# Optimization experiments

Hardware: AMD Instinct MI355X
Metric: run time of the kernel (lower is better)

## Reference

```python
import jax, jax.numpy as jnp
import numpy as np

N_VERTS, N_RADIAL, N_ANGULAR, FEAT = 100000, 5, 8, 16
AMT_TEMPLATES, OUTPUT_DIM = 8, 32


def setup_inputs() -> dict:
    key = jax.random.key(0)
    k1, k2, k3, k4, k5, k6 = jax.random.split(key, 6)
    mesh_signal = jax.random.normal(k1, (N_VERTS, FEAT), dtype=jnp.float32)
    bary_weights = jax.random.uniform(k2, (N_VERTS, N_RADIAL, N_ANGULAR, 3), dtype=jnp.float32)
    interp_coeffs = jax.random.uniform(
        k3, (N_RADIAL, N_ANGULAR, N_RADIAL * N_ANGULAR), dtype=jnp.float32)
    template_weights = jax.random.normal(
        k4, (AMT_TEMPLATES, OUTPUT_DIM, FEAT), dtype=jnp.float32)
    bias = jax.random.normal(k5, (AMT_TEMPLATES, OUTPUT_DIM), dtype=jnp.float32)
    bary_indices = jax.random.randint(k6, (N_VERTS, N_RADIAL, N_ANGULAR, 3), 0, N_VERTS, dtype=jnp.int32)
    return {
        "mesh_signal": mesh_signal,
        "bary_weights": bary_weights,
        "interp_coeffs": interp_coeffs,
        "template_weights": template_weights,
        "bias": bias,
        "bary_indices": bary_indices,
    }


def reference(mesh_signal, bary_weights, interp_coeffs, template_weights, bias, bary_indices):
    n, R, A, _ = bary_indices.shape
    K = R * A
    # --- patch operator: barycentric gather + weighted interpolation ---
    gathered = mesh_signal[bary_indices]                         # (n, R, A, 3, F)
    interp = jnp.einsum('nrak,nrakf->nraf', bary_weights, gathered)  # (n, R, A, F)
    # --- prior: matvec with interpolation coefficients over flattened template ---
    flat = interp.reshape(n, K, -1)                              # (n, K, F)
    interp = jnp.einsum('nkf,rak->nraf', flat, interp_coeffs)    # (n, R, A, F)
    # --- fold: W @ X then reduce_sum over template-vertex axis. Since the
    # activation comes AFTER the reduce_sum, sum(W @ X, -1) == W @ sum(X, -1),
    # so we reduce first to avoid an (n, T, O, K) intermediate. ---
    s = interp.reshape(n, K, -1).sum(axis=1)                     # (n, F)
    pre = jnp.einsum('tof,nf->nto', template_weights, s) + bias  # (n, T, O)
    act = jax.nn.relu(pre)
    return act.sum(axis=1)                                       # (n, O)
```

## Files before the change

kernel.cpp:

```cpp
#include <hip/hip_runtime.h>

#define KK 40
#define M3 120
#define MM4 30
#define RCH 15
#define FEAT 16
#define NT 8
#define ODIM 32
#define VPB 32
#define BLOCK 256
#define SST 17

typedef unsigned int u32;
typedef unsigned short u16;
typedef float  f32x2 __attribute__((ext_vector_type(2)));
typedef float  f32x4 __attribute__((ext_vector_type(4)));
typedef int    i32x4 __attribute__((ext_vector_type(4)));
typedef u32    u32x4 __attribute__((ext_vector_type(4)));

__global__ void cs3_kernel(const float* __restrict__ ic, float* __restrict__ cs3) {
    __shared__ float cs[KK];
    const int t = threadIdx.x;
    if (t < KK) {
        float s = 0.f;
        #pragma unroll
        for (int ra = 0; ra < KK; ++ra) s += ic[ra * KK + t];
        cs[t] = s;
    }
    __syncthreads();
    if (t < M3) cs3[t] = cs[t / 3];
}

__device__ __forceinline__ u16 f2bf_rne(float x) {
    u32 u = __float_as_uint(x);
    u32 r = (u + 0x7fffu + ((u >> 16) & 1u)) >> 16;
    return (u16)r;
}

__global__ void cvt_kernel(const float* __restrict__ mesh, u16* __restrict__ mbf, int total) {
    const int i = blockIdx.x * blockDim.x + threadIdx.x;
    const int base = i * 8;
    if (base < total) {
        f32x4 a = __builtin_nontemporal_load((const f32x4*)(mesh + base));
        f32x4 b = __builtin_nontemporal_load((const f32x4*)(mesh + base + 4));
        u32x4 v;
        v.x = (u32)f2bf_rne(a.x) | ((u32)f2bf_rne(a.y) << 16);
        v.y = (u32)f2bf_rne(a.z) | ((u32)f2bf_rne(a.w) << 16);
        v.z = (u32)f2bf_rne(b.x) | ((u32)f2bf_rne(b.y) << 16);
        v.w = (u32)f2bf_rne(b.z) | ((u32)f2bf_rne(b.w) << 16);
        *(u32x4*)(mbf + base) = v;
    }
}

__device__ __forceinline__ void acc8(f32x2 acc2[4], const u32x4 g, const float s) {
    const f32x2 s2 = {s, s};
    f32x2 p;
    p.x = __uint_as_float(g.x << 16);
    p.y = __uint_as_float(g.x & 0xffff0000u);
    acc2[0] = __builtin_elementwise_fma(p, s2, acc2[0]);
    p.x = __uint_as_float(g.y << 16);
    p.y = __uint_as_float(g.y & 0xffff0000u);
    acc2[1] = __builtin_elementwise_fma(p, s2, acc2[1]);
    p.x = __uint_as_float(g.z << 16);
    p.y = __uint_as_float(g.z & 0xffff0000u);
    acc2[2] = __builtin_elementwise_fma(p, s2, acc2[2]);
    p.x = __uint_as_float(g.w << 16);
    p.y = __uint_as_float(g.w & 0xffff0000u);
    acc2[3] = __builtin_elementwise_fma(p, s2, acc2[3]);
}

__device__ __forceinline__ void gather4_sc0(const u32x4* p0, const u32x4* p1,
                                            const u32x4* p2, const u32x4* p3,
                                            u32x4& g0, u32x4& g1, u32x4& g2, u32x4& g3) {
    asm volatile(
        "global_load_dwordx4 %0, %4, off sc0\n\t"
        "global_load_dwordx4 %1, %5, off sc0\n\t"
        "global_load_dwordx4 %2, %6, off sc0\n\t"
        "global_load_dwordx4 %3, %7, off sc0\n\t"
        "s_waitcnt vmcnt(0)"
        : "=&v"(g0), "=&v"(g1), "=&v"(g2), "=&v"(g3)
        : "v"(p0), "v"(p1), "v"(p2), "v"(p3)
        : "memory");
}

__global__ __launch_bounds__(BLOCK, 8) void conv_kernel(
    const u16*   __restrict__ mbf,
    const float* __restrict__ bw,
    const float* __restrict__ W,
    const float* __restrict__ bias,
    const int*   __restrict__ bi,
    const float* __restrict__ cs3,
    float*       __restrict__ out,
    int n)
{
    __shared__ f32x4 s_buf[VPB * SST * 2];
    __shared__ float s_sig[VPB][FEAT + 1];

    f32x4* s_bw4 = s_buf;
    i32x4* s_bi4 = (i32x4*)(s_buf + VPB * SST);
    float (*s_out)[ODIM + 1] = (float(*)[ODIM + 1])s_buf;

    const int tid = threadIdx.x;
    const int vg0 = blockIdx.x * VPB;

    const f32x4* bw4g  = (const f32x4*)bw;
    const i32x4* bi4g  = (const i32x4*)bi;
    const f32x4* cs34g = (const f32x4*)cs3;

    const int vloc = tid >> 3;
    const int jc   = (tid >> 2) & 1;
    const int mc   = (tid >> 1) & 1;
    const int q    = tid & 1;
    const int vg   = vg0 + vloc;

    f32x2 acc2[4];
    #pragma unroll
    for (int e = 0; e < 4; ++e) acc2[e] = (f32x2){0.f, 0.f};

    #pragma unroll
    for (int r = 0; r < 2; ++r) {
        if (r) __syncthreads();

        #pragma unroll
        for (int ii = 0; ii < 2; ++ii) {
            const int i = tid + ii * BLOCK;
            if (i < VPB * RCH) {
                const int v = i / RCH;
                const int c = i - v * RCH;
                if (vg0 + v < n) {
                    const int gchunk = (vg0 + v) * MM4 + r * RCH + c;
                    f32x4 wv = __builtin_nontemporal_load(bw4g + gchunk);
                    i32x4 iv = __builtin_nontemporal_load(bi4g + gchunk);
                    const f32x4 cc = cs34g[r * RCH + c];
                    wv.x *= cc.x; wv.y *= cc.y; wv.z *= cc.z; wv.w *= cc.w;
                    s_bw4[v * SST + c] = wv;
                    s_bi4[v * SST + c] = iv;
                }
            }
        }
        __syncthreads();

        if (vg < n) {
            const int row   = vloc * SST;
            const int cbase = mc ? 8 : 0;
            #pragma unroll
            for (int b = 0; b < 4; ++b) {
                const int s0 = 2 * b;
                const int s1 = 2 * b + 1;
                const bool v0 = (mc == 0) || (s0 < 7);
                const bool v1 = (mc == 0) || (s1 < 7);
                const f32x4 wq0 = s_bw4[row + (v0 ? cbase + s0 : 0)];
                const i32x4 iq0 = s_bi4[row + (v0 ? cbase + s0 : 0)];
                const f32x4 wq1 = s_bw4[row + (v1 ? cbase + s1 : 0)];
                const i32x4 iq1 = s_bi4[row + (v1 ? cbase + s1 : 0)];
                const float wa0 = v0 ? (jc ? wq0.z : wq0.x) : 0.f;
                const float wa1 = v0 ? (jc ? wq0.w : wq0.y) : 0.f;
                const int   ia0 = v0 ? (jc ? iq0.z : iq0.x) : 0;
                const int   ia1 = v0 ? (jc ? iq0.w : iq0.y) : 0;
                const float wb0 = v1 ? (jc ? wq1.z : wq1.x) : 0.f;
                const float wb1 = v1 ? (jc ? wq1.w : wq1.y) : 0.f;
                const int   ib0 = v1 ? (jc ? iq1.z : iq1.x) : 0;
                const int   ib1 = v1 ? (jc ? iq1.w : iq1.y) : 0;

                u32x4 g0, g1, g2, g3;
                gather4_sc0((const u32x4*)(mbf + (size_t)ia0 * FEAT) + q,
                            (const u32x4*)(mbf + (size_t)ia1 * FEAT) + q,
                            (const u32x4*)(mbf + (size_t)ib0 * FEAT) + q,
                            (const u32x4*)(mbf + (size_t)ib1 * FEAT) + q,
                            g0, g1, g2, g3);

                acc8(acc2, g0, wa0);
                acc8(acc2, g1, wa1);
                acc8(acc2, g2, wb0);
                acc8(acc2, g3, wb1);
            }
        }
    }

    float a8[8] = { acc2[0].x, acc2[0].y, acc2[1].x, acc2[1].y,
                    acc2[2].x, acc2[2].y, acc2[3].x, acc2[3].y };
    #pragma unroll
    for (int e = 0; e < 8; ++e) a8[e] += __shfl_xor(a8[e], 4);
    #pragma unroll
    for (int e = 0; e < 8; ++e) a8[e] += __shfl_xor(a8[e], 2);

    if (jc == 0) {
        const f32x4 v = (mc == 0) ? (f32x4){a8[0], a8[1], a8[2], a8[3]}
                                  : (f32x4){a8[4], a8[5], a8[6], a8[7]};
        *(f32x4*)(&s_sig[vloc][q * 8 + mc * 4]) = v;
    }
    __syncthreads();

    {
        const int lane = tid & 63;
        const int wave = __builtin_amdgcn_readfirstlane(tid >> 6);
        const int v    = lane & (VPB - 1);

        float s[FEAT];
        #pragma unroll
        for (int f = 0; f < FEAT; ++f) s[f] = s_sig[v][f];

        float oacc[8];
        #pragma unroll
        for (int oi = 0; oi < 8; ++oi) oacc[oi] = 0.f;

        #pragma unroll 2
        for (int t = 0; t < NT; ++t) {
            #pragma unroll
            for (int oi = 0; oi < 8; ++oi) {
                const int o = wave * 8 + oi;
                float pre = bias[t * ODIM + o];
                const float* wrow = W + ((size_t)t * ODIM + o) * FEAT;
                #pragma unroll
                for (int f = 0; f < FEAT; ++f)
                    pre = fmaf(wrow[f], s[f], pre);
                oacc[oi] += fmaxf(pre, 0.f);
            }
        }

        if (lane < VPB) {
            #pragma unroll
            for (int oi = 0; oi < 8; ++oi)
                s_out[v][wave * 8 + oi] = oacc[oi];
        }
    }
    __syncthreads();

    {
        const int v   = tid >> 3;
        const int oq  = tid & 7;
        const int vgo = vg0 + v;
        if (vgo < n) {
            const f32x4 val = { s_out[v][oq * 4 + 0], s_out[v][oq * 4 + 1],
                                s_out[v][oq * 4 + 2], s_out[v][oq * 4 + 3] };
            *(f32x4*)(out + (size_t)vgo * ODIM + oq * 4) = val;
        }
    }
}

extern "C" void kernel_launch(void* const* d_in, const int* in_sizes, int n_in,
                              void* d_out, int out_size, void* d_ws, size_t ws_size,
                              hipStream_t stream) {
    const float* mesh = (const float*)d_in[0];
    const float* bw   = (const float*)d_in[1];
    const float* ic   = (const float*)d_in[2];
    const float* W    = (const float*)d_in[3];
    const float* bias = (const float*)d_in[4];
    const int*   bi   = (const int*)d_in[5];
    float* out = (float*)d_out;

    const int n = in_sizes[0] / FEAT;
    const int total = n * FEAT;

    float* cs3 = (float*)d_ws;
    u16*   mbf = (u16*)((char*)d_ws + 512);

    cs3_kernel<<<1, 128, 0, stream>>>(ic, cs3);

    const int cvt_threads = (total + 7) / 8;
    cvt_kernel<<<(cvt_threads + 255) / 256, 256, 0, stream>>>(mesh, mbf, total);

    const int blocks = (n + VPB - 1) / VPB;
    conv_kernel<<<blocks, BLOCK, 0, stream>>>(mbf, bw, W, bias, bi, cs3, out, n);
}
```

Baseline: 93.88 us.

## Software-pipeline gather batches and merge prep kernels into one launch

The gather loop becomes a double-buffered pipeline. Batch N+1 is issued before batch N is consumed, using s_waitcnt vmcnt(4) instead of waiting for all loads to finish, so memory latency overlaps with FMA work. The cs3 and bf16-conversion kernels are merged into one launch to save a kernel launch. Occupancy hint drops from 8 to 6 waves per SIMD to make room for the extra in-flight registers, which may reduce latency hiding across waves.

```diff
diff --git a/kernel.cpp b/kernel.cpp
--- a/kernel.cpp
+++ b/kernel.cpp
@@ -18,27 +18,28 @@
 typedef int    i32x4 __attribute__((ext_vector_type(4)));
 typedef u32    u32x4 __attribute__((ext_vector_type(4)));
 
-__global__ void cs3_kernel(const float* __restrict__ ic, float* __restrict__ cs3) {
-    __shared__ float cs[KK];
-    const int t = threadIdx.x;
-    if (t < KK) {
-        float s = 0.f;
-        #pragma unroll
-        for (int ra = 0; ra < KK; ++ra) s += ic[ra * KK + t];
-        cs[t] = s;
-    }
-    __syncthreads();
-    if (t < M3) cs3[t] = cs[t / 3];
-}
-
 __device__ __forceinline__ u16 f2bf_rne(float x) {
     u32 u = __float_as_uint(x);
     u32 r = (u + 0x7fffu + ((u >> 16) & 1u)) >> 16;
     return (u16)r;
 }
 
-__global__ void cvt_kernel(const float* __restrict__ mesh, u16* __restrict__ mbf, int total) {
-    const int i = blockIdx.x * blockDim.x + threadIdx.x;
+__global__ void prep_kernel(const float* __restrict__ mesh, const float* __restrict__ ic,
+                            u16* __restrict__ mbf, float* __restrict__ cs3, int total) {
+    const int t = threadIdx.x;
+    if (blockIdx.x == 0) {
+        __shared__ float cs[KK];
+        if (t < KK) {
+            float s = 0.f;
+            #pragma unroll
+            for (int ra = 0; ra < KK; ++ra) s += ic[ra * KK + t];
+            cs[t] = s;
+        }
+        __syncthreads();
+        if (t < M3) cs3[t] = cs[t / 3];
+        return;
+    }
+    const int i = (blockIdx.x - 1) * BLOCK + t;
     const int base = i * 8;
     if (base < total) {
         f32x4 a = __builtin_nontemporal_load((const f32x4*)(mesh + base));
@@ -69,21 +70,61 @@
     acc2[3] = __builtin_elementwise_fma(p, s2, acc2[3]);
 }
 
-__device__ __forceinline__ void gather4_sc0(const u32x4* p0, const u32x4* p1,
-                                            const u32x4* p2, const u32x4* p3,
-                                            u32x4& g0, u32x4& g1, u32x4& g2, u32x4& g3) {
+__device__ __forceinline__ void issue4_sc0(const u32x4* p0, const u32x4* p1,
+                                           const u32x4* p2, const u32x4* p3,
+                                           u32x4& g0, u32x4& g1, u32x4& g2, u32x4& g3) {
     asm volatile(
         "global_load_dwordx4 %0, %4, off sc0\n\t"
         "global_load_dwordx4 %1, %5, off sc0\n\t"
         "global_load_dwordx4 %2, %6, off sc0\n\t"
-        "global_load_dwordx4 %3, %7, off sc0\n\t"
-        "s_waitcnt vmcnt(0)"
+        "global_load_dwordx4 %3, %7, off sc0"
         : "=&v"(g0), "=&v"(g1), "=&v"(g2), "=&v"(g3)
         : "v"(p0), "v"(p1), "v"(p2), "v"(p3)
         : "memory");
 }
 
-__global__ __launch_bounds__(BLOCK, 8) void conv_kernel(
+#define WAIT_VM4() do { asm volatile("s_waitcnt vmcnt(4)" ::: "memory"); \
+                        __builtin_amdgcn_sched_barrier(0); } while (0)
+#define WAIT_VM0() do { asm volatile("s_waitcnt vmcnt(0)" ::: "memory"); \
+                        __builtin_amdgcn_sched_barrier(0); } while (0)
+
+struct GBatch { u32x4 g0, g1, g2, g3; float w0, w1, w2, w3; };
+
+__device__ __forceinline__ void prep_issue(GBatch& B,
+                                           const f32x4* __restrict__ s_bw4,
+                                           const i32x4* __restrict__ s_bi4,
+                                           int row, int cbase, int jc, int q, int mc, int b,
+                                           const u16* __restrict__ mbf) {
+    const int s0 = 2 * b, s1 = 2 * b + 1;
+    const bool v0 = (mc == 0) || (s0 < 7);
+    const bool v1 = (mc == 0) || (s1 < 7);
+    const f32x4 wq0 = s_bw4[row + cbase + (v0 ? s0 : 0)];
+    const i32x4 iq0 = s_bi4[row + cbase + (v0 ? s0 : 0)];
+    const f32x4 wq1 = s_bw4[row + cbase + (v1 ? s1 : 0)];
+    const i32x4 iq1 = s_bi4[row + cbase + (v1 ? s1 : 0)];
+    B.w0 = v0 ? (jc ? wq0.z : wq0.x) : 0.f;
+    B.w1 = v0 ? (jc ? wq0.w : wq0.y) : 0.f;
+    B.w2 = v1 ? (jc ? wq1.z : wq1.x) : 0.f;
+    B.w3 = v1 ? (jc ? wq1.w : wq1.y) : 0.f;
+    const int i0 = v0 ? (jc ? iq0.z : iq0.x) : 0;
+    const int i1 = v0 ? (jc ? iq0.w : iq0.y) : 0;
+    const int i2 = v1 ? (jc ? iq1.z : iq1.x) : 0;
+    const int i3 = v1 ? (jc ? iq1.w : iq1.y) : 0;
+    issue4_sc0((const u32x4*)(mbf + (size_t)i0 * FEAT) + q,
+               (const u32x4*)(mbf + (size_t)i1 * FEAT) + q,
+               (const u32x4*)(mbf + (size_t)i2 * FEAT) + q,
+               (const u32x4*)(mbf + (size_t)i3 * FEAT) + q,
+               B.g0, B.g1, B.g2, B.g3);
+}
+
+__device__ __forceinline__ void consume(f32x2 acc2[4], const GBatch& B) {
+    acc8(acc2, B.g0, B.w0);
+    acc8(acc2, B.g1, B.w1);
+    acc8(acc2, B.g2, B.w2);
+    acc8(acc2, B.g3, B.w3);
+}
+
+__global__ __launch_bounds__(BLOCK, 6) void conv_kernel(
     const u16*   __restrict__ mbf,
     const float* __restrict__ bw,
     const float* __restrict__ W,
@@ -143,37 +184,19 @@
         if (vg < n) {
             const int row   = vloc * SST;
             const int cbase = mc ? 8 : 0;
-            #pragma unroll
-            for (int b = 0; b < 4; ++b) {
-                const int s0 = 2 * b;
-                const int s1 = 2 * b + 1;
-                const bool v0 = (mc == 0) || (s0 < 7);
-                const bool v1 = (mc == 0) || (s1 < 7);
-                const f32x4 wq0 = s_bw4[row + (v0 ? cbase + s0 : 0)];
-                const i32x4 iq0 = s_bi4[row + (v0 ? cbase + s0 : 0)];
-                const f32x4 wq1 = s_bw4[row + (v1 ? cbase + s1 : 0)];
-                const i32x4 iq1 = s_bi4[row + (v1 ? cbase + s1 : 0)];
-                const float wa0 = v0 ? (jc ? wq0.z : wq0.x) : 0.f;
-                const float wa1 = v0 ? (jc ? wq0.w : wq0.y) : 0.f;
-                const int   ia0 = v0 ? (jc ? iq0.z : iq0.x) : 0;
-                const int   ia1 = v0 ? (jc ? iq0.w : iq0.y) : 0;
-                const float wb0 = v1 ? (jc ? wq1.z : wq1.x) : 0.f;
-                const float wb1 = v1 ? (jc ? wq1.w : wq1.y) : 0.f;
-                const int   ib0 = v1 ? (jc ? iq1.z : iq1.x) : 0;
-                const int   ib1 = v1 ? (jc ? iq1.w : iq1.y) : 0;
-
-                u32x4 g0, g1, g2, g3;
-                gather4_sc0((const u32x4*)(mbf + (size_t)ia0 * FEAT) + q,
-                            (const u32x4*)(mbf + (size_t)ia1 * FEAT) + q,
-                            (const u32x4*)(mbf + (size_t)ib0 * FEAT) + q,
-                            (const u32x4*)(mbf + (size_t)ib1 * FEAT) + q,
-                            g0, g1, g2, g3);
-
-                acc8(acc2, g0, wa0);
-                acc8(acc2, g1, wa1);
-                acc8(acc2, g2, wb0);
-                acc8(acc2, g3, wb1);
-            }
+            GBatch A, B, C, D;
+            prep_issue(A, s_bw4, s_bi4, row, cbase, jc, q, mc, 0, mbf);
+            prep_issue(B, s_bw4, s_bi4, row, cbase, jc, q, mc, 1, mbf);
+            WAIT_VM4();
+            consume(acc2, A);
+            prep_issue(C, s_bw4, s_bi4, row, cbase, jc, q, mc, 2, mbf);
+            WAIT_VM4();
+            consume(acc2, B);
+            prep_issue(D, s_bw4, s_bi4, row, cbase, jc, q, mc, 3, mbf);
+            WAIT_VM4();
+            consume(acc2, C);
+            WAIT_VM0();
+            consume(acc2, D);
         }
     }
 
@@ -255,10 +278,8 @@
     float* cs3 = (float*)d_ws;
     u16*   mbf = (u16*)((char*)d_ws + 512);
 
-    cs3_kernel<<<1, 128, 0, stream>>>(ic, cs3);
-
-    const int cvt_threads = (total + 7) / 8;
-    cvt_kernel<<<(cvt_threads + 255) / 256, 256, 0, stream>>>(mesh, mbf, total);
+    const int cvt_blocks = (total / 8 + BLOCK - 1) / BLOCK;
+    prep_kernel<<<cvt_blocks + 1, BLOCK, 0, stream>>>(mesh, ic, mbf, cs3, total);
 
     const int blocks = (n + VPB - 1) / VPB;
     conv_kernel<<<blocks, BLOCK, 0, stream>>>(mbf, bw, W, bias, bi, cs3, out, n);
```

After: 86.57 us. 7.8% less time.
